# Kernel optimization log

Hardware: AMD Instinct MI355X
Metric: run time of the kernel (lower is better)

Reference implementation:

```python
import jax, jax.numpy as jnp
import numpy as np

B, T, C, H = 4, 2048, 1024, 16
DK = C // H


def setup_inputs() -> dict:
    key = jax.random.key(0)
    ks = jax.random.split(key, 12)
    s = 1.0 / np.sqrt(C)
    return {
        "q": jax.random.normal(ks[0], (B, T, C), jnp.float32),
        "k": jax.random.normal(ks[1], (B, T, C), jnp.float32),
        "v": jax.random.normal(ks[2], (B, T, C), jnp.float32),
        "mask": jax.random.randint(ks[3], (B, T, T), 0, 2, jnp.int32),
        "Wq": jax.random.normal(ks[4], (C, C), jnp.float32) * s,
        "bq": jnp.zeros((C,), jnp.float32),
        "Wk": jax.random.normal(ks[5], (C, C), jnp.float32) * s,
        "bk": jnp.zeros((C,), jnp.float32),
        "Wv": jax.random.normal(ks[6], (C, C), jnp.float32) * s,
        "bv": jnp.zeros((C,), jnp.float32),
        "Wf": jax.random.normal(ks[7], (C, C), jnp.float32) * s,
        "bf": jnp.zeros((C,), jnp.float32),
    }


def reference(q, k, v, mask, Wq, bq, Wk, bk, Wv, bv, Wf, bf):
    # linear projections (torch Linear: x @ W.T + b), then split heads
    def heads(x, W, b):
        y = x @ W.T + b  # [B,T,C]
        return y.reshape(B, T, H, DK).transpose(0, 2, 1, 3)  # [B,H,T,DK]

    qh, kh, vh = heads(q, Wq, bq), heads(k, Wk, bk), heads(v, Wv, bv)
    att = jnp.einsum("bhqd,bhkd->bhqk", qh, kh) * (1.0 / np.sqrt(DK))
    att = jnp.where(mask[:, None, :, :] == 0, jnp.float32(-1e9), att)
    p = jax.nn.softmax(att, axis=-1)
    y = jnp.einsum("bhqk,bhkd->bhqd", p, vh)  # [B,H,T,DK]
    y = y.transpose(0, 2, 1, 3).reshape(B, T, C)
    return y @ Wf.T + bf
```

## Files before the change

### kernel.cpp

```cpp
#include <hip/hip_runtime.h>

#define B_ 4
#define T_ 2048
#define C_ 1024
#define H_ 16
#define DK_ 64
#define BT_ 8192

using u16 = unsigned short;
using u32 = unsigned int;
using u64 = unsigned long long;
typedef __attribute__((ext_vector_type(8))) short short8;
typedef __attribute__((ext_vector_type(4))) float f32x4;
typedef __attribute__((ext_vector_type(16))) float f32x16;
typedef __attribute__((ext_vector_type(4))) u32 u32x4;
typedef __attribute__((ext_vector_type(2))) u32 u32x2;

__device__ __forceinline__ u16 f2bf(float f) {
  u32 u = __builtin_bit_cast(u32, f);
  u32 r = u + 0x7fffu + ((u >> 16) & 1u);
  return (u16)(r >> 16);
}

__device__ __forceinline__ void glds16(void* lds, const void* g) {
  __builtin_amdgcn_global_load_lds(
      (__attribute__((address_space(1))) u32*)g,
      (__attribute__((address_space(3))) u32*)lds, 16, 0, 0);
}

__device__ __forceinline__ u32 cvtpk_bf16(float lo, float hi) {
  u32 r;
  asm("v_cvt_pk_bf16_f32 %0, %1, %2" : "=v"(r) : "v"(lo), "v"(hi));
  return r;
}

__device__ __forceinline__ void cvt_range(const float* __restrict__ s,
                                          u16* __restrict__ d, int n,
                                          int rb, int nblk) {
  int i0 = (rb * 256 + (int)threadIdx.x) * 4;
  int stride = nblk * 256 * 4;
  for (int i = i0; i < n; i += stride) {
    float4 v = *(const float4*)(s + i);
    u64 p = (u64)f2bf(v.x) | ((u64)f2bf(v.y) << 16) |
            ((u64)f2bf(v.z) << 32) | ((u64)f2bf(v.w) << 48);
    *(u64*)(d + i) = p;
  }
}

__global__ __launch_bounds__(256) void prep_k(
    const float* __restrict__ Wq, const float* __restrict__ Wk,
    const float* __restrict__ Wv, const float* __restrict__ Wf,
    const int* __restrict__ mask,
    u16* __restrict__ Wqb, u16* __restrict__ Wkb, u16* __restrict__ Wvb,
    u16* __restrict__ Wfb, u64* __restrict__ mb) {
  const int bid = blockIdx.x;
  if (bid < 256) {
    const int which = bid >> 6, rb = bid & 63;
    const float* s = which == 0 ? Wq : which == 1 ? Wk : which == 2 ? Wv : Wf;
    u16* d = which == 0 ? Wqb : which == 1 ? Wkb : which == 2 ? Wvb : Wfb;
    cvt_range(s, d, C_ * C_, rb, 64);
  } else {
    const int nch = B_ * T_ * T_ / 256;
    const int lane = threadIdx.x & 63;
    int g0 = (bid - 256) * 16 + ((int)threadIdx.x >> 6) * 4;
    for (int g = g0; g < nch; g += 1792 * 16) {
#pragma unroll
      for (int gg = 0; gg < 4; ++gg) {
        const int4 vv = *(const int4*)(mask + (size_t)(g + gg) * 256 + 4 * lane);
        const u64 b0 = __ballot(vv.x != 0);
        const u64 b1 = __ballot(vv.y != 0);
        const u64 b2 = __ballot(vv.z != 0);
        const u64 b3 = __ballot(vv.w != 0);
        const u64 wv = lane == 0 ? b0 : lane == 1 ? b1 : lane == 2 ? b2 : b3;
        if (lane < 4) mb[(size_t)(g + gg) * 4 + lane] = wv;
      }
    }
  }
}

template <int MODE, int AF, int BF>
__global__ __launch_bounds__(256) void gemm_nt(
    const void* __restrict__ Aa, const void* __restrict__ Ab,
    const void* __restrict__ Ba, const void* __restrict__ Bb,
    const float* __restrict__ biasa, const float* __restrict__ biasb,
    void* __restrict__ outa, void* __restrict__ outb,
    int M, int N, int K, float scalea, float scaleb) {
  __shared__ __align__(16) u16 As[128 * 32];
  __shared__ __align__(16) u16 Bs[128 * 32];
  const void* A = blockIdx.z ? Ab : Aa;
  const void* Bm = blockIdx.z ? Bb : Ba;
  const float* bias = blockIdx.z ? biasb : biasa;
  void* out = blockIdx.z ? outb : outa;
  const float scale = blockIdx.z ? scaleb : scalea;

  const int t = threadIdx.x;
  const int lane = t & 63;
  const int wave = t >> 6;
  const int wr = wave >> 1, wc = wave & 1;
  const int lr = lane & 15, lg = lane >> 4;
  const int m0 = blockIdx.x * 128;
  const int n0 = blockIdx.y * 128;

  f32x4 acc[4][4] = {};

  const int srow = t >> 2;
  const int scol = (t & 3) * 8;
  u16* as0 = &As[srow * 32 + scol];
  u16* as1 = &As[(srow + 64) * 32 + scol];
  u16* bs0 = &Bs[srow * 32 + scol];
  u16* bs1 = &Bs[(srow + 64) * 32 + scol];

  const u16* ag = (const u16*)A + (size_t)(m0 + srow) * K + scol;
  const float* agf = (const float*)A + (size_t)(m0 + srow) * K + scol;
  const u16* bg = (const u16*)Bm + (size_t)(n0 + srow) * K + scol;
  const float* bgf = (const float*)Bm + (size_t)(n0 + srow) * K + scol;

  float4 ax0, ax1, ax2, ax3, bx0, bx1, bx2, bx3;
  if (AF) {
    ax0 = *(const float4*)(agf);
    ax1 = *(const float4*)(agf + 4);
    ax2 = *(const float4*)(agf + (size_t)64 * K);
    ax3 = *(const float4*)(agf + (size_t)64 * K + 4);
  }
  if (BF) {
    bx0 = *(const float4*)(bgf);
    bx1 = *(const float4*)(bgf + 4);
    bx2 = *(const float4*)(bgf + (size_t)64 * K);
    bx3 = *(const float4*)(bgf + (size_t)64 * K + 4);
  }

  for (int k0 = 0; k0 < K; k0 += 32) {
    if (AF) {
      const u32x4 p0 = {cvtpk_bf16(ax0.x, ax0.y), cvtpk_bf16(ax0.z, ax0.w),
                        cvtpk_bf16(ax1.x, ax1.y), cvtpk_bf16(ax1.z, ax1.w)};
      const u32x4 p1 = {cvtpk_bf16(ax2.x, ax2.y), cvtpk_bf16(ax2.z, ax2.w),
                        cvtpk_bf16(ax3.x, ax3.y), cvtpk_bf16(ax3.z, ax3.w)};
      *(u32x4*)as0 = p0;
      *(u32x4*)as1 = p1;
      if (k0 + 32 < K) {
        ax0 = *(const float4*)(agf + k0 + 32);
        ax1 = *(const float4*)(agf + k0 + 36);
        ax2 = *(const float4*)(agf + (size_t)64 * K + k0 + 32);
        ax3 = *(const float4*)(agf + (size_t)64 * K + k0 + 36);
      }
    } else {
      glds16(as0, ag + k0);
      glds16(as1, ag + (size_t)64 * K + k0);
    }
    if (BF) {
      const u32x4 p0 = {cvtpk_bf16(bx0.x, bx0.y), cvtpk_bf16(bx0.z, bx0.w),
                        cvtpk_bf16(bx1.x, bx1.y), cvtpk_bf16(bx1.z, bx1.w)};
      const u32x4 p1 = {cvtpk_bf16(bx2.x, bx2.y), cvtpk_bf16(bx2.z, bx2.w),
                        cvtpk_bf16(bx3.x, bx3.y), cvtpk_bf16(bx3.z, bx3.w)};
      *(u32x4*)bs0 = p0;
      *(u32x4*)bs1 = p1;
      if (k0 + 32 < K) {
        bx0 = *(const float4*)(bgf + k0 + 32);
        bx1 = *(const float4*)(bgf + k0 + 36);
        bx2 = *(const float4*)(bgf + (size_t)64 * K + k0 + 32);
        bx3 = *(const float4*)(bgf + (size_t)64 * K + k0 + 36);
      }
    } else {
      glds16(bs0, bg + k0);
      glds16(bs1, bg + (size_t)64 * K + k0);
    }
    __syncthreads();
    short8 af[4], bf[4];
#pragma unroll
    for (int m = 0; m < 4; ++m)
      af[m] = *(const short8*)&As[(wr * 64 + m * 16 + lr) * 32 + lg * 8];
#pragma unroll
    for (int n = 0; n < 4; ++n)
      bf[n] = *(const short8*)&Bs[(wc * 64 + n * 16 + lr) * 32 + lg * 8];
#pragma unroll
    for (int m = 0; m < 4; ++m)
#pragma unroll
      for (int n = 0; n < 4; ++n)
        acc[m][n] = __builtin_amdgcn_mfma_f32_16x16x32_bf16(af[m], bf[n], acc[m][n], 0, 0, 0);
    __syncthreads();
  }

#pragma unroll
  for (int m = 0; m < 4; ++m) {
#pragma unroll
    for (int n = 0; n < 4; ++n) {
#pragma unroll
      for (int j = 0; j < 4; ++j) {
        const int gm = m0 + wr * 64 + m * 16 + lg * 4 + j;
        const int gn = n0 + wc * 64 + n * 16 + lr;
        float v = acc[m][n][j];
        if (MODE == 0) {
          v = (v + bias[gn]) * scale;
          const int b = gm >> 11, tt = gm & 2047, h = gn >> 6, d = gn & 63;
          ((u16*)out)[((((size_t)b * H_ + h) * T_ + tt) << 6) + d] = f2bf(v);
        } else if (MODE == 1) {
          v += bias[gm];
          const int gnp = (gn & ~12) | ((gn & 4) << 1) | ((gn & 8) >> 1);
          ((u16*)out)[(size_t)gm * N + gnp] = f2bf(v);
        } else {
          v += bias[gn];
          ((float*)out)[(size_t)gm * N + gn] = v;
        }
      }
    }
  }
}

__global__ __launch_bounds__(512) void attn32_k(
    const u16* __restrict__ Qh, const u16* __restrict__ Kh,
    const u16* __restrict__ Vt, const u64* __restrict__ mb,
    u16* __restrict__ Y) {
  __shared__ __align__(16) u16 Ks[2][128 * 68];
  __shared__ __align__(16) u16 Vs[2][64 * 132];

  const int f = blockIdx.x;
  const int lgid = ((f & 7) << 6) | (f >> 3);
  const int bh = lgid >> 3, qblk = lgid & 7;
  const int b = bh >> 4, h = bh & 15;
  const int t = threadIdx.x;
  const int wave = t >> 6, lane = t & 63;
  const int lq = lane & 31, hi = lane >> 5;
  const int q0 = qblk * 256 + wave * 32;

  const u16* Qp = Qh + ((size_t)bh * T_ + q0 + lq) * DK_ + hi * 8;
  short8 qf[4];
#pragma unroll
  for (int kt = 0; kt < 4; ++kt) qf[kt] = *(const short8*)(Qp + kt * 16);

  const u16* KgB = Kh + (size_t)bh * T_ * DK_;
  const u16* VtB = Vt + (size_t)h * DK_ * BT_ + (size_t)b * T_;
  const u64* mrow = mb + ((size_t)b * T_ + q0 + lq) * (T_ / 64);

  const int kr = t >> 3, ku = t & 7;
  const u16* ksrcA = KgB + (size_t)kr * DK_ + ku * 8;
  const u16* ksrcB = KgB + (size_t)(kr + 64) * DK_ + ku * 8;
  const int kdstA = kr * 68 + ku * 8, kdstB = (kr + 64) * 68 + ku * 8;
  const int vr = t >> 4, vu = t & 15;
  const u16* vsrcA = VtB + (size_t)vr * BT_ + vu * 8;
  const u16* vsrcB = VtB + (size_t)(vr + 32) * BT_ + vu * 8;
  const int vdstA = vr * 132 + vu * 8, vdstB = (vr + 32) * 132 + vu * 8;

  const u32x4 onesu = {0x3F803F80u, 0x3F803F80u, 0x3F803F80u, 0x3F803F80u};
  const short8 ones8 = __builtin_bit_cast(short8, onesu);

  f32x16 o0 = {}, o1 = {}, accl = {};

  u32x4 kpA = *(const u32x4*)(ksrcA), kpB = *(const u32x4*)(ksrcB);
  u32x4 vpA = *(const u32x4*)(vsrcA), vpB = *(const u32x4*)(vsrcB);
  *(u32x2*)&Ks[0][kdstA] = (u32x2){kpA[0], kpA[1]};
  *(u32x2*)&Ks[0][kdstA + 4] = (u32x2){kpA[2], kpA[3]};
  *(u32x2*)&Ks[0][kdstB] = (u32x2){kpB[0], kpB[1]};
  *(u32x2*)&Ks[0][kdstB + 4] = (u32x2){kpB[2], kpB[3]};
  *(u32x2*)&Vs[0][vdstA] = (u32x2){vpA[0], vpA[1]};
  *(u32x2*)&Vs[0][vdstA + 4] = (u32x2){vpA[2], vpA[3]};
  *(u32x2*)&Vs[0][vdstB] = (u32x2){vpB[0], vpB[1]};
  *(u32x2*)&Vs[0][vdstB + 4] = (u32x2){vpB[2], vpB[3]};
  __syncthreads();
  int cur = 0;

  for (int kv = 0; kv < T_; kv += 128) {
    const bool pre = (kv + 128) < T_;
    if (pre) {
      kpA = *(const u32x4*)(ksrcA + (size_t)(kv + 128) * DK_);
      kpB = *(const u32x4*)(ksrcB + (size_t)(kv + 128) * DK_);
      vpA = *(const u32x4*)(vsrcA + (kv + 128));
      vpB = *(const u32x4*)(vsrcB + (kv + 128));
    }

#pragma unroll
    for (int s2 = 0; s2 < 2; ++s2) {
      const int kvs = kv + 64 * s2;
      f32x16 c0 = {}, c1 = {};
      __builtin_amdgcn_s_setprio(1);
#pragma unroll
      for (int kt = 0; kt < 4; ++kt) {
        const int ix = (2 * kt + hi) * 8;
        const u32x2 a0 = *(const u32x2*)&Ks[cur][(64 * s2 + lq) * 68 + ix];
        const u32x2 a1 = *(const u32x2*)&Ks[cur][(64 * s2 + lq) * 68 + ix + 4];
        const u32x2 b0 = *(const u32x2*)&Ks[cur][(64 * s2 + lq + 32) * 68 + ix];
        const u32x2 b1 = *(const u32x2*)&Ks[cur][(64 * s2 + lq + 32) * 68 + ix + 4];
        const u32x4 k0u = {a0[0], a0[1], a1[0], a1[1]};
        const u32x4 k1u = {b0[0], b0[1], b1[0], b1[1]};
        c0 = __builtin_amdgcn_mfma_f32_32x32x16_bf16(
            __builtin_bit_cast(short8, k0u), qf[kt], c0, 0, 0, 0);
        c1 = __builtin_amdgcn_mfma_f32_32x32x16_bf16(
            __builtin_bit_cast(short8, k1u), qf[kt], c1, 0, 0, 0);
      }
      __builtin_amdgcn_s_setprio(0);

      const u64* wp = mrow + ((kvs >> 8) << 2);
      const int sh = ((kvs >> 2) & 48) + hi;
      u32 tp[4];
#pragma unroll
      for (int e = 0; e < 4; ++e) tp[e] = (u32)(wp[e] >> sh);
#pragma unroll
      for (int r = 0; r < 16; ++r) {
        const int pp = 2 * (r >> 2);
        const u32 k0m = (u32)(((int)(tp[r & 3] << (31 - pp))) >> 31);
        const u32 k1m = (u32)(((int)(tp[r & 3] << (23 - pp))) >> 31);
        c0[r] = __builtin_bit_cast(
            float, __builtin_bit_cast(u32, __builtin_amdgcn_exp2f(c0[r])) & k0m);
        c1[r] = __builtin_bit_cast(
            float, __builtin_bit_cast(u32, __builtin_amdgcn_exp2f(c1[r])) & k1m);
      }

      u32 pw_[4][4];
#pragma unroll
      for (int g = 0; g < 4; ++g) {
        const int ob = (g & 1) * 8;
#pragma unroll
        for (int w2 = 0; w2 < 4; ++w2) {
          const float lo = (g < 2) ? c0[ob + 2 * w2] : c1[ob + 2 * w2];
          const float hii = (g < 2) ? c0[ob + 2 * w2 + 1] : c1[ob + 2 * w2 + 1];
          pw_[g][w2] = cvtpk_bf16(lo, hii);
        }
      }

      __builtin_amdgcn_s_setprio(1);
#pragma unroll
      for (int g = 0; g < 4; ++g) {
        const int ix = 16 * (4 * s2 + g) + 8 * hi;
        const u32x2 va = *(const u32x2*)&Vs[cur][lq * 132 + ix];
        const u32x2 vb = *(const u32x2*)&Vs[cur][lq * 132 + ix + 4];
        const u32x2 wa = *(const u32x2*)&Vs[cur][(lq + 32) * 132 + ix];
        const u32x2 wb = *(const u32x2*)&Vs[cur][(lq + 32) * 132 + ix + 4];
        const u32x4 pu = {pw_[g][0], pw_[g][1], pw_[g][2], pw_[g][3]};
        const u32x4 v0u = {va[0], va[1], vb[0], vb[1]};
        const u32x4 v1u = {wa[0], wa[1], wb[0], wb[1]};
        const short8 pa = __builtin_bit_cast(short8, pu);
        o0 = __builtin_amdgcn_mfma_f32_32x32x16_bf16(
            pa, __builtin_bit_cast(short8, v0u), o0, 0, 0, 0);
        o1 = __builtin_amdgcn_mfma_f32_32x32x16_bf16(
            pa, __builtin_bit_cast(short8, v1u), o1, 0, 0, 0);
        accl = __builtin_amdgcn_mfma_f32_32x32x16_bf16(pa, ones8, accl, 0, 0, 0);
      }
      __builtin_amdgcn_s_setprio(0);
    }

    if (pre) {
      *(u32x2*)&Ks[cur ^ 1][kdstA] = (u32x2){kpA[0], kpA[1]};
      *(u32x2*)&Ks[cur ^ 1][kdstA + 4] = (u32x2){kpA[2], kpA[3]};
      *(u32x2*)&Ks[cur ^ 1][kdstB] = (u32x2){kpB[0], kpB[1]};
      *(u32x2*)&Ks[cur ^ 1][kdstB + 4] = (u32x2){kpB[2], kpB[3]};
      *(u32x2*)&Vs[cur ^ 1][vdstA] = (u32x2){vpA[0], vpA[1]};
      *(u32x2*)&Vs[cur ^ 1][vdstA + 4] = (u32x2){vpA[2], vpA[3]};
      *(u32x2*)&Vs[cur ^ 1][vdstB] = (u32x2){vpB[0], vpB[1]};
      *(u32x2*)&Vs[cur ^ 1][vdstB + 4] = (u32x2){vpB[2], vpB[3]};
    }
    __syncthreads();
    cur ^= 1;
  }

#pragma unroll
  for (int r = 0; r < 16; ++r) {
    const int row = (r & 3) + 8 * (r >> 2) + 4 * hi;
    const float li = 1.0f / accl[r];
    u16* yp = Y + ((size_t)b * T_ + q0 + row) * C_ + h * DK_ + lq;
    yp[0] = f2bf(o0[r] * li);
    yp[32] = f2bf(o1[r] * li);
  }
}

extern "C" void kernel_launch(void* const* d_in, const int* in_sizes, int n_in,
                              void* d_out, int out_size, void* d_ws, size_t ws_size,
                              hipStream_t stream) {
  const float* q  = (const float*)d_in[0];
  const float* k  = (const float*)d_in[1];
  const float* v  = (const float*)d_in[2];
  const int* mask = (const int*)d_in[3];
  const float* Wq = (const float*)d_in[4];
  const float* bq = (const float*)d_in[5];
  const float* Wk = (const float*)d_in[6];
  const float* bk = (const float*)d_in[7];
  const float* Wv = (const float*)d_in[8];
  const float* bv = (const float*)d_in[9];
  const float* Wf = (const float*)d_in[10];
  const float* bf = (const float*)d_in[11];
  float* out = (float*)d_out;
  char* ws = (char*)d_ws;

  size_t off = 0;
  auto nxt = [&](size_t bytes) -> void* {
    void* p = ws + off;
    off += (bytes + 255) & ~(size_t)255;
    return p;
  };
  const size_t big = (size_t)BT_ * C_ * 2;
  const size_t wsz = (size_t)C_ * C_ * 2;
  u16* Wqb = (u16*)nxt(wsz);
  u16* Wkb = (u16*)nxt(wsz);
  u16* Wvb = (u16*)nxt(wsz);
  u16* Wfb = (u16*)nxt(wsz);
  u16* Qh  = (u16*)nxt(big);
  u16* Kh  = (u16*)nxt(big);
  u16* Vt  = (u16*)nxt(big);
  u16* Yb  = (u16*)nxt(big);
  u64* mb  = (u64*)nxt((size_t)B_ * T_ * (T_ / 64) * 8);

  prep_k<<<2048, 256, 0, stream>>>(Wq, Wk, Wv, Wf, mask,
                                   Wqb, Wkb, Wvb, Wfb, mb);

  const float qscale = 0.125f * 1.4426950408889634f;
  gemm_nt<0, 1, 0><<<dim3(BT_ / 128, C_ / 128, 2), 256, 0, stream>>>(
      q, k, Wqb, Wkb, bq, bk, Qh, Kh, BT_, C_, C_, qscale, 1.0f);
  gemm_nt<1, 0, 1><<<dim3(C_ / 128, BT_ / 128, 1), 256, 0, stream>>>(
      Wvb, Wvb, v, v, bv, bv, Vt, Vt, C_, BT_, C_, 1.0f, 1.0f);

  attn32_k<<<B_ * H_ * (T_ / 256), 512, 0, stream>>>(Qh, Kh, Vt, mb, Yb);

  gemm_nt<2, 0, 0><<<dim3(BT_ / 128, C_ / 128, 1), 256, 0, stream>>>(
      Yb, Yb, Wfb, Wfb, bf, bf, out, out, BT_, C_, C_, 1.0f, 1.0f);
}
```

Before: 278.1 us.

## Pre-convert activations to bf16 and merge QKV projections with mask packing

The prep kernel now converts the q, k and v activations to bf16 up front along with the weights. The Q/K and V projection GEMMs, plus the mask bit-packing, are merged into a single launch with four z-slices. Every projection now loads tiles through the direct-to-LDS path instead of converting fp32 in registers, and one launch is removed. In exchange it writes and re-reads three extra bf16 activation buffers in global memory, and the mask packing now competes with the GEMM blocks inside the same grid.

Result: faster. 270.5 us (-2.7%).

```diff
diff --git a/kernel.cpp b/kernel.cpp
--- a/kernel.cpp
+++ b/kernel.cpp
@@ -48,22 +48,48 @@
 }
 
 __global__ __launch_bounds__(256) void prep_k(
-    const float* __restrict__ Wq, const float* __restrict__ Wk,
-    const float* __restrict__ Wv, const float* __restrict__ Wf,
-    const int* __restrict__ mask,
+    const float* __restrict__ q, const float* __restrict__ k,
+    const float* __restrict__ v, const float* __restrict__ Wq,
+    const float* __restrict__ Wk, const float* __restrict__ Wv,
+    const float* __restrict__ Wf,
+    u16* __restrict__ qb, u16* __restrict__ kb, u16* __restrict__ vb,
     u16* __restrict__ Wqb, u16* __restrict__ Wkb, u16* __restrict__ Wvb,
-    u16* __restrict__ Wfb, u64* __restrict__ mb) {
+    u16* __restrict__ Wfb) {
   const int bid = blockIdx.x;
-  if (bid < 256) {
-    const int which = bid >> 6, rb = bid & 63;
+  if (bid < 1890) {
+    const int which = bid / 630, rb = bid % 630;
+    const float* s = which == 0 ? q : which == 1 ? k : v;
+    u16* d = which == 0 ? qb : which == 1 ? kb : vb;
+    cvt_range(s, d, BT_ * C_, rb, 630);
+  } else if (bid < 2046) {
+    const int idx = bid - 1890;
+    const int which = idx / 39, rb = idx % 39;
     const float* s = which == 0 ? Wq : which == 1 ? Wk : which == 2 ? Wv : Wf;
     u16* d = which == 0 ? Wqb : which == 1 ? Wkb : which == 2 ? Wvb : Wfb;
-    cvt_range(s, d, C_ * C_, rb, 64);
-  } else {
+    cvt_range(s, d, C_ * C_, rb, 39);
+  }
+}
+
+__global__ __launch_bounds__(256) void proj_k(
+    const u16* __restrict__ qb, const u16* __restrict__ kb,
+    const u16* __restrict__ vb,
+    const u16* __restrict__ Wqb, const u16* __restrict__ Wkb,
+    const u16* __restrict__ Wvb,
+    const float* __restrict__ bq, const float* __restrict__ bk,
+    const float* __restrict__ bv,
+    u16* __restrict__ Qh, u16* __restrict__ Kh, u16* __restrict__ Vt,
+    const int* __restrict__ mask, u64* __restrict__ mb, float qscale) {
+  __shared__ __align__(16) u16 As[128 * 32];
+  __shared__ __align__(16) u16 Bs[128 * 32];
+  const int z = blockIdx.z;
+  const int t = threadIdx.x;
+
+  if (z == 3) {
+    const int fid = blockIdx.y * 64 + blockIdx.x;
+    const int lane = t & 63;
     const int nch = B_ * T_ * T_ / 256;
-    const int lane = threadIdx.x & 63;
-    int g0 = (bid - 256) * 16 + ((int)threadIdx.x >> 6) * 4;
-    for (int g = g0; g < nch; g += 1792 * 16) {
+    int g0 = fid * 16 + (t >> 6) * 4;
+    for (int g = g0; g < nch; g += 512 * 16) {
 #pragma unroll
       for (int gg = 0; gg < 4; ++gg) {
         const int4 vv = *(const int4*)(mask + (size_t)(g + gg) * 256 + 4 * lane);
@@ -75,24 +101,85 @@
         if (lane < 4) mb[(size_t)(g + gg) * 4 + lane] = wv;
       }
     }
-  }
-}
-
-template <int MODE, int AF, int BF>
-__global__ __launch_bounds__(256) void gemm_nt(
-    const void* __restrict__ Aa, const void* __restrict__ Ab,
-    const void* __restrict__ Ba, const void* __restrict__ Bb,
-    const float* __restrict__ biasa, const float* __restrict__ biasb,
-    void* __restrict__ outa, void* __restrict__ outb,
-    int M, int N, int K, float scalea, float scaleb) {
+    return;
+  }
+
+  const u16* A = z == 0 ? qb : z == 1 ? kb : Wvb;
+  const u16* Bm = z == 0 ? Wqb : z == 1 ? Wkb : vb;
+  const float* bias = z == 0 ? bq : z == 1 ? bk : bv;
+  u16* out = z == 0 ? Qh : z == 1 ? Kh : Vt;
+  const float scale = z == 0 ? qscale : 1.0f;
+  const int m0 = (z == 2 ? blockIdx.y : blockIdx.x) * 128;
+  const int n0 = (z == 2 ? blockIdx.x : blockIdx.y) * 128;
+  const int N = z == 2 ? BT_ : C_;
+  const int K = C_;
+
+  const int lane = t & 63;
+  const int wave = t >> 6;
+  const int wr = wave >> 1, wc = wave & 1;
+  const int lr = lane & 15, lg = lane >> 4;
+
+  f32x4 acc[4][4] = {};
+
+  const int srow = t >> 2;
+  const int scol = (t & 3) * 8;
+  const u16* ag = A + (size_t)(m0 + srow) * K + scol;
+  const u16* bg = Bm + (size_t)(n0 + srow) * K + scol;
+  u16* as0 = &As[srow * 32 + scol];
+  u16* as1 = &As[(srow + 64) * 32 + scol];
+  u16* bs0 = &Bs[srow * 32 + scol];
+  u16* bs1 = &Bs[(srow + 64) * 32 + scol];
+
+  for (int k0 = 0; k0 < K; k0 += 32) {
+    glds16(as0, ag + k0);
+    glds16(as1, ag + (size_t)64 * K + k0);
+    glds16(bs0, bg + k0);
+    glds16(bs1, bg + (size_t)64 * K + k0);
+    __syncthreads();
+    short8 af[4], bf[4];
+#pragma unroll
+    for (int m = 0; m < 4; ++m)
+      af[m] = *(const short8*)&As[(wr * 64 + m * 16 + lr) * 32 + lg * 8];
+#pragma unroll
+    for (int n = 0; n < 4; ++n)
+      bf[n] = *(const short8*)&Bs[(wc * 64 + n * 16 + lr) * 32 + lg * 8];
+#pragma unroll
+    for (int m = 0; m < 4; ++m)
+#pragma unroll
+      for (int n = 0; n < 4; ++n)
+        acc[m][n] = __builtin_amdgcn_mfma_f32_16x16x32_bf16(af[m], bf[n], acc[m][n], 0, 0, 0);
+    __syncthreads();
+  }
+
+#pragma unroll
+  for (int m = 0; m < 4; ++m) {
+#pragma unroll
+    for (int n = 0; n < 4; ++n) {
+#pragma unroll
+      for (int j = 0; j < 4; ++j) {
+        const int gm = m0 + wr * 64 + m * 16 + lg * 4 + j;
+        const int gn = n0 + wc * 64 + n * 16 + lr;
+        float v = acc[m][n][j];
+        if (z <= 1) {
+          v = (v + bias[gn]) * scale;
+          const int b = gm >> 11, tt = gm & 2047, h = gn >> 6, d = gn & 63;
+          out[((((size_t)b * H_ + h) * T_ + tt) << 6) + d] = f2bf(v);
+        } else {
+          v += bias[gm];
+          const int gnp = (gn & ~12) | ((gn & 4) << 1) | ((gn & 8) >> 1);
+          out[(size_t)gm * N + gnp] = f2bf(v);
+        }
+      }
+    }
+  }
+}
+
+__global__ __launch_bounds__(256) void out_k(
+    const u16* __restrict__ A, const u16* __restrict__ Bm,
+    const float* __restrict__ bias, float* __restrict__ out,
+    int M, int N, int K) {
   __shared__ __align__(16) u16 As[128 * 32];
   __shared__ __align__(16) u16 Bs[128 * 32];
-  const void* A = blockIdx.z ? Ab : Aa;
-  const void* Bm = blockIdx.z ? Bb : Ba;
-  const float* bias = blockIdx.z ? biasb : biasa;
-  void* out = blockIdx.z ? outb : outa;
-  const float scale = blockIdx.z ? scaleb : scalea;
-
   const int t = threadIdx.x;
   const int lane = t & 63;
   const int wave = t >> 6;
@@ -105,65 +192,18 @@
 
   const int srow = t >> 2;
   const int scol = (t & 3) * 8;
+  const u16* ag = A + (size_t)(m0 + srow) * K + scol;
+  const u16* bg = Bm + (size_t)(n0 + srow) * K + scol;
   u16* as0 = &As[srow * 32 + scol];
   u16* as1 = &As[(srow + 64) * 32 + scol];
   u16* bs0 = &Bs[srow * 32 + scol];
   u16* bs1 = &Bs[(srow + 64) * 32 + scol];
 
-  const u16* ag = (const u16*)A + (size_t)(m0 + srow) * K + scol;
-  const float* agf = (const float*)A + (size_t)(m0 + srow) * K + scol;
-  const u16* bg = (const u16*)Bm + (size_t)(n0 + srow) * K + scol;
-  const float* bgf = (const float*)Bm + (size_t)(n0 + srow) * K + scol;
-
-  float4 ax0, ax1, ax2, ax3, bx0, bx1, bx2, bx3;
-  if (AF) {
-    ax0 = *(const float4*)(agf);
-    ax1 = *(const float4*)(agf + 4);
-    ax2 = *(const float4*)(agf + (size_t)64 * K);
-    ax3 = *(const float4*)(agf + (size_t)64 * K + 4);
-  }
-  if (BF) {
-    bx0 = *(const float4*)(bgf);
-    bx1 = *(const float4*)(bgf + 4);
-    bx2 = *(const float4*)(bgf + (size_t)64 * K);
-    bx3 = *(const float4*)(bgf + (size_t)64 * K + 4);
-  }
-
   for (int k0 = 0; k0 < K; k0 += 32) {
-    if (AF) {
-      const u32x4 p0 = {cvtpk_bf16(ax0.x, ax0.y), cvtpk_bf16(ax0.z, ax0.w),
-                        cvtpk_bf16(ax1.x, ax1.y), cvtpk_bf16(ax1.z, ax1.w)};
-      const u32x4 p1 = {cvtpk_bf16(ax2.x, ax2.y), cvtpk_bf16(ax2.z, ax2.w),
-                        cvtpk_bf16(ax3.x, ax3.y), cvtpk_bf16(ax3.z, ax3.w)};
-      *(u32x4*)as0 = p0;
-      *(u32x4*)as1 = p1;
-      if (k0 + 32 < K) {
-        ax0 = *(const float4*)(agf + k0 + 32);
-        ax1 = *(const float4*)(agf + k0 + 36);
-        ax2 = *(const float4*)(agf + (size_t)64 * K + k0 + 32);
-        ax3 = *(const float4*)(agf + (size_t)64 * K + k0 + 36);
-      }
-    } else {
-      glds16(as0, ag + k0);
-      glds16(as1, ag + (size_t)64 * K + k0);
-    }
-    if (BF) {
-      const u32x4 p0 = {cvtpk_bf16(bx0.x, bx0.y), cvtpk_bf16(bx0.z, bx0.w),
-                        cvtpk_bf16(bx1.x, bx1.y), cvtpk_bf16(bx1.z, bx1.w)};
-      const u32x4 p1 = {cvtpk_bf16(bx2.x, bx2.y), cvtpk_bf16(bx2.z, bx2.w),
-                        cvtpk_bf16(bx3.x, bx3.y), cvtpk_bf16(bx3.z, bx3.w)};
-      *(u32x4*)bs0 = p0;
-      *(u32x4*)bs1 = p1;
-      if (k0 + 32 < K) {
-        bx0 = *(const float4*)(bgf + k0 + 32);
-        bx1 = *(const float4*)(bgf + k0 + 36);
-        bx2 = *(const float4*)(bgf + (size_t)64 * K + k0 + 32);
-        bx3 = *(const float4*)(bgf + (size_t)64 * K + k0 + 36);
-      }
-    } else {
-      glds16(bs0, bg + k0);
-      glds16(bs1, bg + (size_t)64 * K + k0);
-    }
+    glds16(as0, ag + k0);
+    glds16(as1, ag + (size_t)64 * K + k0);
+    glds16(bs0, bg + k0);
+    glds16(bs1, bg + (size_t)64 * K + k0);
     __syncthreads();
     short8 af[4], bf[4];
 #pragma unroll
@@ -181,29 +221,15 @@
   }
 
 #pragma unroll
-  for (int m = 0; m < 4; ++m) {
-#pragma unroll
-    for (int n = 0; n < 4; ++n) {
+  for (int m = 0; m < 4; ++m)
+#pragma unroll
+    for (int n = 0; n < 4; ++n)
 #pragma unroll
       for (int j = 0; j < 4; ++j) {
         const int gm = m0 + wr * 64 + m * 16 + lg * 4 + j;
         const int gn = n0 + wc * 64 + n * 16 + lr;
-        float v = acc[m][n][j];
-        if (MODE == 0) {
-          v = (v + bias[gn]) * scale;
-          const int b = gm >> 11, tt = gm & 2047, h = gn >> 6, d = gn & 63;
-          ((u16*)out)[((((size_t)b * H_ + h) * T_ + tt) << 6) + d] = f2bf(v);
-        } else if (MODE == 1) {
-          v += bias[gm];
-          const int gnp = (gn & ~12) | ((gn & 4) << 1) | ((gn & 8) >> 1);
-          ((u16*)out)[(size_t)gm * N + gnp] = f2bf(v);
-        } else {
-          v += bias[gn];
-          ((float*)out)[(size_t)gm * N + gn] = v;
-        }
-      }
-    }
-  }
+        out[(size_t)gm * N + gn] = acc[m][n][j] + bias[gn];
+      }
 }
 
 __global__ __launch_bounds__(512) void attn32_k(
@@ -387,6 +413,9 @@
   };
   const size_t big = (size_t)BT_ * C_ * 2;
   const size_t wsz = (size_t)C_ * C_ * 2;
+  u16* qb  = (u16*)nxt(big);
+  u16* kb  = (u16*)nxt(big);
+  u16* vb  = (u16*)nxt(big);
   u16* Wqb = (u16*)nxt(wsz);
   u16* Wkb = (u16*)nxt(wsz);
   u16* Wvb = (u16*)nxt(wsz);
@@ -397,17 +426,15 @@
   u16* Yb  = (u16*)nxt(big);
   u64* mb  = (u64*)nxt((size_t)B_ * T_ * (T_ / 64) * 8);
 
-  prep_k<<<2048, 256, 0, stream>>>(Wq, Wk, Wv, Wf, mask,
-                                   Wqb, Wkb, Wvb, Wfb, mb);
+  prep_k<<<2048, 256, 0, stream>>>(q, k, v, Wq, Wk, Wv, Wf,
+                                   qb, kb, vb, Wqb, Wkb, Wvb, Wfb);
 
   const float qscale = 0.125f * 1.4426950408889634f;
-  gemm_nt<0, 1, 0><<<dim3(BT_ / 128, C_ / 128, 2), 256, 0, stream>>>(
-      q, k, Wqb, Wkb, bq, bk, Qh, Kh, BT_, C_, C_, qscale, 1.0f);
-  gemm_nt<1, 0, 1><<<dim3(C_ / 128, BT_ / 128, 1), 256, 0, stream>>>(
-      Wvb, Wvb, v, v, bv, bv, Vt, Vt, C_, BT_, C_, 1.0f, 1.0f);
+  proj_k<<<dim3(64, 8, 4), 256, 0, stream>>>(
+      qb, kb, vb, Wqb, Wkb, Wvb, bq, bk, bv, Qh, Kh, Vt, mask, mb, qscale);
 
   attn32_k<<<B_ * H_ * (T_ / 256), 512, 0, stream>>>(Qh, Kh, Vt, mb, Yb);
 
-  gemm_nt<2, 0, 0><<<dim3(BT_ / 128, C_ / 128, 1), 256, 0, stream>>>(
-      Yb, Yb, Wfb, Wfb, bf, bf, out, out, BT_, C_, C_, 1.0f, 1.0f);
-}
+  out_k<<<dim3(BT_ / 128, C_ / 128), 256, 0, stream>>>(
+      Yb, Wfb, bf, out, BT_, C_, C_);
+}
```
